# Kernel optimization log

Hardware: AMD Instinct MI355X
Metric: run time of the kernel (lower is better)

The kernel has to match this reference:

```python
import jax, jax.numpy as jnp
import numpy as np

EPS = 1e-12  # matches tf.nn.l2_normalize epsilon used by keras backend


def l2n(x, axis):
    return x / jnp.sqrt(jnp.maximum(jnp.sum(x * x, axis=axis, keepdims=True), EPS))


def setup_inputs() -> dict:
    key = jax.random.key(0)
    k1, k2, k3 = jax.random.split(key, 3)
    B, T, D, P = 32, 256, 512, 20
    inp_a = jax.random.normal(k1, (B, T, D), dtype=jnp.float32)
    inp_b = jax.random.normal(k2, (B, T, D), dtype=jnp.float32)
    # build(): output_dim weights of shape (1, D), 'uniform' init -> stacked (P, D)
    W = jax.random.uniform(k3, (P, D), dtype=jnp.float32, minval=-0.05, maxval=0.05)
    return {"inp_a": inp_a, "inp_b": inp_b, "W": W}


def reference(inp_a, inp_b, W):
    # l2-normalize over feature dim
    na = l2n(inp_a, -1)  # (B,T,D)
    nb = l2n(inp_b, -1)  # (B,T,D)
    # K.batch_dot(outp_b, outp_a, axes=[1,1]): contract seq axis -> (B,D,D)
    alpha = jnp.einsum('btd,bte->bde', nb, na)
    alpha = l2n(alpha, 1)
    # K.batch_dot(outp_b, alpha, axes=[2,1]): contract feature axis of b with axis1 of alpha -> (B,T,D)
    hmean = jnp.einsum('btd,bde->bte', nb, alpha)
    # per-perspective weighting + l2-normalize, vectorized over P perspectives
    aw = l2n(inp_a[:, :, None, :] * W[None, None, :, :], -1)   # (B,T,P,D)
    hw = l2n(hmean[:, :, None, :] * W[None, None, :, :], -1)   # (B,T,P,D)
    # batch_dot(hw_i, aw_i, axes=[2,2]) * eye summed == rowwise dot (diagonal only)
    persp = jnp.sum(aw * hw, axis=-1)  # (B,T,P)
    return (persp, persp)
```

## Files before the change

kernel.cpp:

```cpp
#include <hip/hip_runtime.h>
#include <hip/hip_bf16.h>

#define BB 32
#define TT 256
#define DD 512
#define PP 20
#define EPSF 1e-12f
#define BTP (BB * TT * PP)

typedef __attribute__((ext_vector_type(8))) short short8;
typedef __attribute__((ext_vector_type(4))) float f32x4;

__device__ inline unsigned short f2bf(float f) {
    unsigned u = __float_as_uint(f);
    u += 0x7fffu + ((u >> 16) & 1u);
    return (unsigned short)(u >> 16);
}
__device__ inline unsigned pk2(float lo, float hi) {
    __hip_bfloat162 h = __float22bfloat162_rn(float2{lo, hi});
    union { __hip_bfloat162 h; unsigned u; } c;
    c.h = h;
    return c.u;
}
__device__ inline float bf2f(unsigned s) {
    return __uint_as_float(s << 16);
}

union U8 { short8 s; uint4 u; };

__global__ __launch_bounds__(256)
void k_prep(const float* __restrict__ a, const float* __restrict__ b,
            const float* __restrict__ W,
            unsigned short* __restrict__ na_bf,
            unsigned short* __restrict__ nb_bf,
            float* __restrict__ q, unsigned short* __restrict__ W2) {
    const int row  = blockIdx.x * 4 + (threadIdx.x >> 6);
    const int lane = threadIdx.x & 63;
    const float4* pa = (const float4*)(a + (size_t)row * DD);
    const float4* pb = (const float4*)(b + (size_t)row * DD);
    float4 a0 = pa[2 * lane], a1 = pa[2 * lane + 1];
    float4 b0 = pb[2 * lane], b1 = pb[2 * lane + 1];
    float sa = a0.x * a0.x + a0.y * a0.y + a0.z * a0.z + a0.w * a0.w
             + a1.x * a1.x + a1.y * a1.y + a1.z * a1.z + a1.w * a1.w;
    float sb = b0.x * b0.x + b0.y * b0.y + b0.z * b0.z + b0.w * b0.w
             + b1.x * b1.x + b1.y * b1.y + b1.z * b1.z + b1.w * b1.w;
#pragma unroll
    for (int off = 1; off < 64; off <<= 1) {
        sa += __shfl_xor(sa, off);
        sb += __shfl_xor(sb, off);
    }
    const float ia_ = rsqrtf(fmaxf(sa, EPSF));
    const float ib_ = rsqrtf(fmaxf(sb, EPSF));
    uint4 oa, ob;
    oa.x = pk2(a0.x * ia_, a0.y * ia_);
    oa.y = pk2(a0.z * ia_, a0.w * ia_);
    oa.z = pk2(a1.x * ia_, a1.y * ia_);
    oa.w = pk2(a1.z * ia_, a1.w * ia_);
    ob.x = pk2(b0.x * ib_, b0.y * ib_);
    ob.y = pk2(b0.z * ib_, b0.w * ib_);
    ob.z = pk2(b1.x * ib_, b1.y * ib_);
    ob.w = pk2(b1.z * ib_, b1.w * ib_);
    *(uint4*)(na_bf + (size_t)row * DD + 8 * lane) = oa;
    *(uint4*)(nb_bf + (size_t)row * DD + 8 * lane) = ob;
    if (lane < 2) {
        const int i2 = 2 * row + lane;
        q[i2] = 0.f;
        const float w = (i2 < PP * DD) ? W[i2] : 0.f;
        W2[i2] = f2bf(w * w);
    }
}

__global__ __launch_bounds__(256)
void k_gemm_g(const unsigned short* __restrict__ nb,
              unsigned short* __restrict__ G) {
    const int bz  = blockIdx.z;
    const int tid = threadIdx.x;
    const int t0 = blockIdx.y * 64;
    const int s0 = blockIdx.x * 64;
    __shared__ __align__(16) unsigned short As[64 * 40];
    __shared__ __align__(16) unsigned short Bs[64 * 40];

    const int wave = tid >> 6, lane = tid & 63;
    const int quad = lane >> 4, ln = lane & 15;
    const int wm = wave >> 1, wn = wave & 1;

    const unsigned short* nbb = nb + (size_t)bz * TT * DD;

    const int lr = tid >> 2;
    const int c8 = (tid & 3) * 8;

    f32x4 acc[2][2];
#pragma unroll
    for (int i = 0; i < 2; ++i)
#pragma unroll
        for (int j = 0; j < 2; ++j)
#pragma unroll
            for (int r = 0; r < 4; ++r) acc[i][j][r] = 0.f;

    for (int k0 = 0; k0 < DD; k0 += 32) {
        *(uint4*)&As[lr * 40 + c8] =
            *(const uint4*)(nbb + (size_t)(t0 + lr) * DD + k0 + c8);
        *(uint4*)&Bs[lr * 40 + c8] =
            *(const uint4*)(nbb + (size_t)(s0 + lr) * DD + k0 + c8);
        __syncthreads();
        short8 af[2], bf[2];
        af[0] = *(const short8*)&As[(wm * 32 + ln) * 40 + quad * 8];
        af[1] = *(const short8*)&As[(wm * 32 + 16 + ln) * 40 + quad * 8];
        bf[0] = *(const short8*)&Bs[(wn * 32 + ln) * 40 + quad * 8];
        bf[1] = *(const short8*)&Bs[(wn * 32 + 16 + ln) * 40 + quad * 8];
#pragma unroll
        for (int i = 0; i < 2; ++i)
#pragma unroll
            for (int j = 0; j < 2; ++j)
                acc[i][j] = __builtin_amdgcn_mfma_f32_16x16x32_bf16(
                    af[i], bf[j], acc[i][j], 0, 0, 0);
        __syncthreads();
    }
    unsigned short* Gb = G + (size_t)bz * TT * TT;
#pragma unroll
    for (int i = 0; i < 2; ++i)
#pragma unroll
        for (int j = 0; j < 2; ++j) {
            const int col = s0 + wn * 32 + j * 16 + ln;
            const int row0 = t0 + wm * 32 + i * 16 + quad * 4;
#pragma unroll
            for (int r = 0; r < 4; r += 2) {
                const unsigned pk = pk2(acc[i][j][r], acc[i][j][r + 1]);
                Gb[(size_t)(row0 + r) * TT + col] = (unsigned short)pk;
                Gb[(size_t)(row0 + r + 1) * TT + col] = (unsigned short)(pk >> 16);
            }
        }
}

__global__ __launch_bounds__(256)
void k_gemm_h(const unsigned short* __restrict__ G,
              const unsigned short* __restrict__ na,
              unsigned short* __restrict__ H, float* __restrict__ q) {
    const int bz = blockIdx.z;
    const int t0 = blockIdx.y * 64;
    const int e0 = blockIdx.x * 64;
    __shared__ __align__(16) unsigned short As[64 * 40];
    __shared__ __align__(16) unsigned short Bs[64 * 40];
    __shared__ float qsum[64];

    const int tid  = threadIdx.x;
    const int wave = tid >> 6, lane = tid & 63;
    const int quad = lane >> 4, ln = lane & 15;
    const int wm = wave >> 1, wn = wave & 1;

    const unsigned short* Gb  = G  + (size_t)bz * TT * TT;
    const unsigned short* nab = na + (size_t)bz * TT * DD;

    const int lr = tid >> 2;
    const int c8 = (tid & 3) * 8;
    const int kr = tid >> 3;
    const int e8 = (tid & 7) * 8;

    f32x4 acc[2][2];
#pragma unroll
    for (int i = 0; i < 2; ++i)
#pragma unroll
        for (int j = 0; j < 2; ++j)
#pragma unroll
            for (int r = 0; r < 4; ++r) acc[i][j][r] = 0.f;

    for (int k0 = 0; k0 < TT; k0 += 32) {
        *(uint4*)&As[lr * 40 + c8] =
            *(const uint4*)(Gb + (size_t)(t0 + lr) * TT + k0 + c8);
        {
            uint4 v = *(const uint4*)(nab + (size_t)(k0 + kr) * DD + e0 + e8);
            Bs[(e8 + 0) * 40 + kr] = (unsigned short)(v.x);
            Bs[(e8 + 1) * 40 + kr] = (unsigned short)(v.x >> 16);
            Bs[(e8 + 2) * 40 + kr] = (unsigned short)(v.y);
            Bs[(e8 + 3) * 40 + kr] = (unsigned short)(v.y >> 16);
            Bs[(e8 + 4) * 40 + kr] = (unsigned short)(v.z);
            Bs[(e8 + 5) * 40 + kr] = (unsigned short)(v.z >> 16);
            Bs[(e8 + 6) * 40 + kr] = (unsigned short)(v.w);
            Bs[(e8 + 7) * 40 + kr] = (unsigned short)(v.w >> 16);
        }
        __syncthreads();
        short8 af[2], bf[2];
        af[0] = *(const short8*)&As[(wm * 32 + ln) * 40 + quad * 8];
        af[1] = *(const short8*)&As[(wm * 32 + 16 + ln) * 40 + quad * 8];
        bf[0] = *(const short8*)&Bs[(wn * 32 + ln) * 40 + quad * 8];
        bf[1] = *(const short8*)&Bs[(wn * 32 + 16 + ln) * 40 + quad * 8];
#pragma unroll
        for (int i = 0; i < 2; ++i)
#pragma unroll
            for (int j = 0; j < 2; ++j)
                acc[i][j] = __builtin_amdgcn_mfma_f32_16x16x32_bf16(
                    af[i], bf[j], acc[i][j], 0, 0, 0);
        __syncthreads();
    }

    if (tid < 64) qsum[tid] = 0.f;
    __syncthreads();

    unsigned short* Hb = H + (size_t)bz * TT * DD;
#pragma unroll
    for (int j = 0; j < 2; ++j) {
        const int col = e0 + wn * 32 + j * 16 + ln;
        float qp = 0.f;
#pragma unroll
        for (int i = 0; i < 2; ++i) {
            const int row0 = t0 + wm * 32 + i * 16 + quad * 4;
#pragma unroll
            for (int r = 0; r < 4; r += 2) {
                const float hv0 = acc[i][j][r];
                const float hv1 = acc[i][j][r + 1];
                const unsigned pk = pk2(hv0, hv1);
                Hb[(size_t)(row0 + r) * DD + col] = (unsigned short)pk;
                Hb[(size_t)(row0 + r + 1) * DD + col] = (unsigned short)(pk >> 16);
                qp = fmaf(bf2f(nab[(size_t)(row0 + r) * DD + col]), hv0, qp);
                qp = fmaf(bf2f(nab[(size_t)(row0 + r + 1) * DD + col]), hv1, qp);
            }
        }
        qp += __shfl_xor(qp, 16);
        qp += __shfl_xor(qp, 32);
        if (quad == 0) atomicAdd(&qsum[wn * 32 + j * 16 + ln], qp);
    }
    __syncthreads();
    if (tid < 64) atomicAdd(q + bz * DD + e0 + tid, qsum[tid]);
}

__global__ __launch_bounds__(128)
void k_persp_mfma(const unsigned short* __restrict__ na,
                  const unsigned short* __restrict__ H,
                  const float* __restrict__ q,
                  const unsigned short* __restrict__ W2,
                  float* __restrict__ out) {
    const int b    = blockIdx.y;
    const int r0   = blockIdx.x * 16;
    const int wave = threadIdx.x >> 6;
    const int lane = threadIdx.x & 63;
    const int quad = lane >> 4, ln = lane & 15;
    const size_t rowbase = ((size_t)b * TT + r0 + ln) * DD;

    __shared__ float qs[DD];
    __shared__ float ps[64][24];
    {
        const float* qb = q + (size_t)b * DD;
        float4 v = *(const float4*)(qb + 4 * threadIdx.x);
        qs[4 * threadIdx.x + 0] = rsqrtf(fmaxf(v.x, EPSF));
        qs[4 * threadIdx.x + 1] = rsqrtf(fmaxf(v.y, EPSF));
        qs[4 * threadIdx.x + 2] = rsqrtf(fmaxf(v.z, EPSF));
        qs[4 * threadIdx.x + 3] = rsqrtf(fmaxf(v.w, EPSF));
    }
    __syncthreads();

    f32x4 s1[2], s2[2], s3[2];
#pragma unroll
    for (int j = 0; j < 2; ++j)
#pragma unroll
        for (int r = 0; r < 4; ++r) { s1[j][r] = 0.f; s2[j][r] = 0.f; s3[j][r] = 0.f; }

    const int kbeg = wave * 256;
    for (int k0 = kbeg; k0 < kbeg + 256; k0 += 32) {
        const int k = k0 + quad * 8;
        uint4 au = *(const uint4*)(na + rowbase + k);
        uint4 hu = *(const uint4*)(H + rowbase + k);
        float4 q0 = *(const float4*)&qs[k];
        float4 q1 = *(const float4*)&qs[k + 4];
        const float av[8] = {bf2f(au.x & 0xffffu), bf2f(au.x >> 16),
                             bf2f(au.y & 0xffffu), bf2f(au.y >> 16),
                             bf2f(au.z & 0xffffu), bf2f(au.z >> 16),
                             bf2f(au.w & 0xffffu), bf2f(au.w >> 16)};
        const float qv[8] = {q0.x, q0.y, q0.z, q0.w, q1.x, q1.y, q1.z, q1.w};
        float hv[8] = {bf2f(hu.x & 0xffffu), bf2f(hu.x >> 16),
                       bf2f(hu.y & 0xffffu), bf2f(hu.y >> 16),
                       bf2f(hu.z & 0xffffu), bf2f(hu.z >> 16),
                       bf2f(hu.w & 0xffffu), bf2f(hu.w >> 16)};
#pragma unroll
        for (int t = 0; t < 8; ++t) hv[t] *= qv[t];
        U8 ah, aa, hh;
        ah.u.x = pk2(av[0] * hv[0], av[1] * hv[1]);
        ah.u.y = pk2(av[2] * hv[2], av[3] * hv[3]);
        ah.u.z = pk2(av[4] * hv[4], av[5] * hv[5]);
        ah.u.w = pk2(av[6] * hv[6], av[7] * hv[7]);
        aa.u.x = pk2(av[0] * av[0], av[1] * av[1]);
        aa.u.y = pk2(av[2] * av[2], av[3] * av[3]);
        aa.u.z = pk2(av[4] * av[4], av[5] * av[5]);
        aa.u.w = pk2(av[6] * av[6], av[7] * av[7]);
        hh.u.x = pk2(hv[0] * hv[0], hv[1] * hv[1]);
        hh.u.y = pk2(hv[2] * hv[2], hv[3] * hv[3]);
        hh.u.z = pk2(hv[4] * hv[4], hv[5] * hv[5]);
        hh.u.w = pk2(hv[6] * hv[6], hv[7] * hv[7]);
        short8 bw0 = *(const short8*)(W2 + (size_t)ln * DD + k);
        short8 bw1 = *(const short8*)(W2 + (size_t)(16 + ln) * DD + k);
        s1[0] = __builtin_amdgcn_mfma_f32_16x16x32_bf16(ah.s, bw0, s1[0], 0, 0, 0);
        s1[1] = __builtin_amdgcn_mfma_f32_16x16x32_bf16(ah.s, bw1, s1[1], 0, 0, 0);
        s2[0] = __builtin_amdgcn_mfma_f32_16x16x32_bf16(aa.s, bw0, s2[0], 0, 0, 0);
        s2[1] = __builtin_amdgcn_mfma_f32_16x16x32_bf16(aa.s, bw1, s2[1], 0, 0, 0);
        s3[0] = __builtin_amdgcn_mfma_f32_16x16x32_bf16(hh.s, bw0, s3[0], 0, 0, 0);
        s3[1] = __builtin_amdgcn_mfma_f32_16x16x32_bf16(hh.s, bw1, s3[1], 0, 0, 0);
    }

    if (wave == 1) {
#pragma unroll
        for (int j = 0; j < 2; ++j)
#pragma unroll
            for (int r = 0; r < 4; ++r) {
                ps[lane][j * 4 + r]      = s1[j][r];
                ps[lane][8 + j * 4 + r]  = s2[j][r];
                ps[lane][16 + j * 4 + r] = s3[j][r];
            }
    }
    __syncthreads();
    if (wave == 0) {
#pragma unroll
        for (int j = 0; j < 2; ++j) {
            const int p = j * 16 + ln;
            if (p < PP) {
#pragma unroll
                for (int r = 0; r < 4; ++r) {
                    const float v1 = s1[j][r] + ps[lane][j * 4 + r];
                    const float v2 = s2[j][r] + ps[lane][8 + j * 4 + r];
                    const float v3 = s3[j][r] + ps[lane][16 + j * 4 + r];
                    const size_t row = (size_t)b * TT + r0 + quad * 4 + r;
                    const float v = v1 * rsqrtf(fmaxf(v2, EPSF))
                                       * rsqrtf(fmaxf(v3, EPSF));
                    out[row * PP + p] = v;
                    out[(size_t)BTP + row * PP + p] = v;
                }
            }
        }
    }
}

extern "C" void kernel_launch(void* const* d_in, const int* in_sizes, int n_in,
                              void* d_out, int out_size, void* d_ws, size_t ws_size,
                              hipStream_t stream) {
    (void)in_sizes; (void)n_in; (void)out_size; (void)ws_size;
    const float* a = (const float*)d_in[0];
    const float* b = (const float*)d_in[1];
    const float* W = (const float*)d_in[2];
    float* out = (float*)d_out;

    char* ws = (char*)d_ws;
    unsigned short* nb_bf = (unsigned short*)ws;
    unsigned short* na_bf = (unsigned short*)(ws + (8u << 20));
    unsigned short* G_bf  = (unsigned short*)(ws + (16u << 20));
    unsigned short* H_bf  = (unsigned short*)(ws + (20u << 20));
    float* q     = (float*)(ws + (28u << 20));
    unsigned short* W2 = (unsigned short*)(ws + (28u << 20) + (64u << 10));

    k_prep<<<BB * TT / 4, 256, 0, stream>>>(a, b, W, na_bf, nb_bf, q, W2);

    dim3 gG(4, 4, BB);
    k_gemm_g<<<gG, 256, 0, stream>>>(nb_bf, G_bf);

    dim3 gH(DD / 64, TT / 64, BB);
    k_gemm_h<<<gH, 256, 0, stream>>>(G_bf, na_bf, H_bf, q);

    dim3 gP(TT / 16, BB);
    k_persp_mfma<<<gP, 128, 0, stream>>>(na_bf, H_bf, q, W2, out);
}
```

Before: 111.7 us.

## Fuse four kernels into one cooperative persistent kernel with grid syncs

Merges the prep, two GEMM, and perspective kernels into a single cooperative kernel of 256 blocks. Grid-wide syncs replace the kernel boundaries, and each block loops over several tiles per phase. The aim is to remove three launch gaps and their tail effects. In exchange, parallelism drops to 256 blocks, which may underuse the 256 CUs with little latency hiding, and each grid.sync adds barrier cost.

New measurement: 235.5 us. +110.8%, slower.

```diff
diff --git a/kernel.cpp b/kernel.cpp
--- a/kernel.cpp
+++ b/kernel.cpp
@@ -1,5 +1,8 @@
 #include <hip/hip_runtime.h>
 #include <hip/hip_bf16.h>
+#include <hip/hip_cooperative_groups.h>
+
+namespace cg = cooperative_groups;
 
 #define BB 32
 #define TT 256
@@ -28,299 +31,308 @@
 
 union U8 { short8 s; uint4 u; };
 
+union SMem {
+    struct {
+        unsigned short As[64 * 40];
+        unsigned short Bs[64 * 40];
+        float qsum[64];
+    } g;
+    struct {
+        float qs[DD];
+        float ps[2][64][24];
+    } p;
+};
+
 __global__ __launch_bounds__(256)
-void k_prep(const float* __restrict__ a, const float* __restrict__ b,
+void k_mega(const float* __restrict__ a, const float* __restrict__ b,
             const float* __restrict__ W,
             unsigned short* __restrict__ na_bf,
             unsigned short* __restrict__ nb_bf,
-            float* __restrict__ q, unsigned short* __restrict__ W2) {
-    const int row  = blockIdx.x * 4 + (threadIdx.x >> 6);
-    const int lane = threadIdx.x & 63;
-    const float4* pa = (const float4*)(a + (size_t)row * DD);
-    const float4* pb = (const float4*)(b + (size_t)row * DD);
-    float4 a0 = pa[2 * lane], a1 = pa[2 * lane + 1];
-    float4 b0 = pb[2 * lane], b1 = pb[2 * lane + 1];
-    float sa = a0.x * a0.x + a0.y * a0.y + a0.z * a0.z + a0.w * a0.w
-             + a1.x * a1.x + a1.y * a1.y + a1.z * a1.z + a1.w * a1.w;
-    float sb = b0.x * b0.x + b0.y * b0.y + b0.z * b0.z + b0.w * b0.w
-             + b1.x * b1.x + b1.y * b1.y + b1.z * b1.z + b1.w * b1.w;
-#pragma unroll
-    for (int off = 1; off < 64; off <<= 1) {
-        sa += __shfl_xor(sa, off);
-        sb += __shfl_xor(sb, off);
+            unsigned short* __restrict__ G,
+            unsigned short* __restrict__ H,
+            float* __restrict__ q, unsigned short* __restrict__ W2,
+            float* __restrict__ out) {
+    __shared__ __align__(16) SMem sm;
+    cg::grid_group grid = cg::this_grid();
+
+    const int tid  = threadIdx.x;
+    const int wave = tid >> 6;
+    const int lane = tid & 63;
+    const int quad = lane >> 4, ln = lane & 15;
+
+    {
+        const int w = blockIdx.x * 4 + wave;
+#pragma unroll
+        for (int r8 = 0; r8 < 8; ++r8) {
+            const int row = w * 8 + r8;
+            const float4* pa = (const float4*)(a + (size_t)row * DD);
+            const float4* pb = (const float4*)(b + (size_t)row * DD);
+            float4 a0 = pa[2 * lane], a1 = pa[2 * lane + 1];
+            float4 b0 = pb[2 * lane], b1 = pb[2 * lane + 1];
+            float sa = a0.x * a0.x + a0.y * a0.y + a0.z * a0.z + a0.w * a0.w
+                     + a1.x * a1.x + a1.y * a1.y + a1.z * a1.z + a1.w * a1.w;
+            float sb = b0.x * b0.x + b0.y * b0.y + b0.z * b0.z + b0.w * b0.w
+                     + b1.x * b1.x + b1.y * b1.y + b1.z * b1.z + b1.w * b1.w;
+#pragma unroll
+            for (int off = 1; off < 64; off <<= 1) {
+                sa += __shfl_xor(sa, off);
+                sb += __shfl_xor(sb, off);
+            }
+            const float ia_ = rsqrtf(fmaxf(sa, EPSF));
+            const float ib_ = rsqrtf(fmaxf(sb, EPSF));
+            uint4 oa, ob;
+            oa.x = pk2(a0.x * ia_, a0.y * ia_);
+            oa.y = pk2(a0.z * ia_, a0.w * ia_);
+            oa.z = pk2(a1.x * ia_, a1.y * ia_);
+            oa.w = pk2(a1.z * ia_, a1.w * ia_);
+            ob.x = pk2(b0.x * ib_, b0.y * ib_);
+            ob.y = pk2(b0.z * ib_, b0.w * ib_);
+            ob.z = pk2(b1.x * ib_, b1.y * ib_);
+            ob.w = pk2(b1.z * ib_, b1.w * ib_);
+            *(uint4*)(na_bf + (size_t)row * DD + 8 * lane) = oa;
+            *(uint4*)(nb_bf + (size_t)row * DD + 8 * lane) = ob;
+            if (lane < 2) {
+                const int i2 = 2 * row + lane;
+                q[i2] = 0.f;
+                const float w2 = (i2 < PP * DD) ? W[i2] : 0.f;
+                W2[i2] = f2bf(w2 * w2);
+            }
+        }
     }
-    const float ia_ = rsqrtf(fmaxf(sa, EPSF));
-    const float ib_ = rsqrtf(fmaxf(sb, EPSF));
-    uint4 oa, ob;
-    oa.x = pk2(a0.x * ia_, a0.y * ia_);
-    oa.y = pk2(a0.z * ia_, a0.w * ia_);
-    oa.z = pk2(a1.x * ia_, a1.y * ia_);
-    oa.w = pk2(a1.z * ia_, a1.w * ia_);
-    ob.x = pk2(b0.x * ib_, b0.y * ib_);
-    ob.y = pk2(b0.z * ib_, b0.w * ib_);
-    ob.z = pk2(b1.x * ib_, b1.y * ib_);
-    ob.w = pk2(b1.z * ib_, b1.w * ib_);
-    *(uint4*)(na_bf + (size_t)row * DD + 8 * lane) = oa;
-    *(uint4*)(nb_bf + (size_t)row * DD + 8 * lane) = ob;
-    if (lane < 2) {
-        const int i2 = 2 * row + lane;
-        q[i2] = 0.f;
-        const float w = (i2 < PP * DD) ? W[i2] : 0.f;
-        W2[i2] = f2bf(w * w);
+    grid.sync();
+
+    {
+        const int wm = wave >> 1, wn = wave & 1;
+        const int lr = tid >> 2;
+        const int c8 = (tid & 3) * 8;
+#pragma unroll
+        for (int it = 0; it < 2; ++it) {
+            const int tt = blockIdx.x * 2 + it;
+            const int bz = tt >> 4;
+            const int t0 = ((tt >> 2) & 3) * 64;
+            const int s0 = (tt & 3) * 64;
+            const unsigned short* nbb = nb_bf + (size_t)bz * TT * DD;
+
+            f32x4 acc[2][2];
+#pragma unroll
+            for (int i = 0; i < 2; ++i)
+#pragma unroll
+                for (int j = 0; j < 2; ++j)
+#pragma unroll
+                    for (int r = 0; r < 4; ++r) acc[i][j][r] = 0.f;
+
+            for (int k0 = 0; k0 < DD; k0 += 32) {
+                *(uint4*)&sm.g.As[lr * 40 + c8] =
+                    *(const uint4*)(nbb + (size_t)(t0 + lr) * DD + k0 + c8);
+                *(uint4*)&sm.g.Bs[lr * 40 + c8] =
+                    *(const uint4*)(nbb + (size_t)(s0 + lr) * DD + k0 + c8);
+                __syncthreads();
+                short8 af[2], bf[2];
+                af[0] = *(const short8*)&sm.g.As[(wm * 32 + ln) * 40 + quad * 8];
+                af[1] = *(const short8*)&sm.g.As[(wm * 32 + 16 + ln) * 40 + quad * 8];
+                bf[0] = *(const short8*)&sm.g.Bs[(wn * 32 + ln) * 40 + quad * 8];
+                bf[1] = *(const short8*)&sm.g.Bs[(wn * 32 + 16 + ln) * 40 + quad * 8];
+#pragma unroll
+                for (int i = 0; i < 2; ++i)
+#pragma unroll
+                    for (int j = 0; j < 2; ++j)
+                        acc[i][j] = __builtin_amdgcn_mfma_f32_16x16x32_bf16(
+                            af[i], bf[j], acc[i][j], 0, 0, 0);
+                __syncthreads();
+            }
+            unsigned short* Gb = G + (size_t)bz * TT * TT;
+#pragma unroll
+            for (int i = 0; i < 2; ++i)
+#pragma unroll
+                for (int j = 0; j < 2; ++j) {
+                    const int col = s0 + wn * 32 + j * 16 + ln;
+                    const int row0 = t0 + wm * 32 + i * 16 + quad * 4;
+#pragma unroll
+                    for (int r = 0; r < 4; r += 2) {
+                        const unsigned pk = pk2(acc[i][j][r], acc[i][j][r + 1]);
+                        Gb[(size_t)(row0 + r) * TT + col] = (unsigned short)pk;
+                        Gb[(size_t)(row0 + r + 1) * TT + col] = (unsigned short)(pk >> 16);
+                    }
+                }
+        }
     }
-}
-
-__global__ __launch_bounds__(256)
-void k_gemm_g(const unsigned short* __restrict__ nb,
-              unsigned short* __restrict__ G) {
-    const int bz  = blockIdx.z;
-    const int tid = threadIdx.x;
-    const int t0 = blockIdx.y * 64;
-    const int s0 = blockIdx.x * 64;
-    __shared__ __align__(16) unsigned short As[64 * 40];
-    __shared__ __align__(16) unsigned short Bs[64 * 40];
-
-    const int wave = tid >> 6, lane = tid & 63;
-    const int quad = lane >> 4, ln = lane & 15;
-    const int wm = wave >> 1, wn = wave & 1;
-
-    const unsigned short* nbb = nb + (size_t)bz * TT * DD;
-
-    const int lr = tid >> 2;
-    const int c8 = (tid & 3) * 8;
-
-    f32x4 acc[2][2];
-#pragma unroll
-    for (int i = 0; i < 2; ++i)
+    grid.sync();
+
+    {
+        const int wm = wave >> 1, wn = wave & 1;
+        const int lr = tid >> 2;
+        const int c8 = (tid & 3) * 8;
+        const int kr = tid >> 3;
+        const int e8 = (tid & 7) * 8;
+#pragma unroll
+        for (int it = 0; it < 4; ++it) {
+            const int tt = blockIdx.x * 4 + it;
+            const int bz = tt >> 5;
+            const int t0 = ((tt >> 3) & 3) * 64;
+            const int e0 = (tt & 7) * 64;
+            const unsigned short* Gb  = G     + (size_t)bz * TT * TT;
+            const unsigned short* nab = na_bf + (size_t)bz * TT * DD;
+
+            f32x4 acc[2][2];
+#pragma unroll
+            for (int i = 0; i < 2; ++i)
+#pragma unroll
+                for (int j = 0; j < 2; ++j)
+#pragma unroll
+                    for (int r = 0; r < 4; ++r) acc[i][j][r] = 0.f;
+
+            for (int k0 = 0; k0 < TT; k0 += 32) {
+                *(uint4*)&sm.g.As[lr * 40 + c8] =
+                    *(const uint4*)(Gb + (size_t)(t0 + lr) * TT + k0 + c8);
+                {
+                    uint4 v = *(const uint4*)(nab + (size_t)(k0 + kr) * DD + e0 + e8);
+                    sm.g.Bs[(e8 + 0) * 40 + kr] = (unsigned short)(v.x);
+                    sm.g.Bs[(e8 + 1) * 40 + kr] = (unsigned short)(v.x >> 16);
+                    sm.g.Bs[(e8 + 2) * 40 + kr] = (unsigned short)(v.y);
+                    sm.g.Bs[(e8 + 3) * 40 + kr] = (unsigned short)(v.y >> 16);
+                    sm.g.Bs[(e8 + 4) * 40 + kr] = (unsigned short)(v.z);
+                    sm.g.Bs[(e8 + 5) * 40 + kr] = (unsigned short)(v.z >> 16);
+                    sm.g.Bs[(e8 + 6) * 40 + kr] = (unsigned short)(v.w);
+                    sm.g.Bs[(e8 + 7) * 40 + kr] = (unsigned short)(v.w >> 16);
+                }
+                __syncthreads();
+                short8 af[2], bf[2];
+                af[0] = *(const short8*)&sm.g.As[(wm * 32 + ln) * 40 + quad * 8];
+                af[1] = *(const short8*)&sm.g.As[(wm * 32 + 16 + ln) * 40 + quad * 8];
+                bf[0] = *(const short8*)&sm.g.Bs[(wn * 32 + ln) * 40 + quad * 8];
+                bf[1] = *(const short8*)&sm.g.Bs[(wn * 32 + 16 + ln) * 40 + quad * 8];
+#pragma unroll
+                for (int i = 0; i < 2; ++i)
+#pragma unroll
+                    for (int j = 0; j < 2; ++j)
+                        acc[i][j] = __builtin_amdgcn_mfma_f32_16x16x32_bf16(
+                            af[i], bf[j], acc[i][j], 0, 0, 0);
+                __syncthreads();
+            }
+
+            if (tid < 64) sm.g.qsum[tid] = 0.f;
+            __syncthreads();
+
+            unsigned short* Hb = H + (size_t)bz * TT * DD;
+#pragma unroll
+            for (int j = 0; j < 2; ++j) {
+                const int col = e0 + wn * 32 + j * 16 + ln;
+                float qp = 0.f;
+#pragma unroll
+                for (int i = 0; i < 2; ++i) {
+                    const int row0 = t0 + wm * 32 + i * 16 + quad * 4;
+#pragma unroll
+                    for (int r = 0; r < 4; r += 2) {
+                        const float hv0 = acc[i][j][r];
+                        const float hv1 = acc[i][j][r + 1];
+                        const unsigned pk = pk2(hv0, hv1);
+                        Hb[(size_t)(row0 + r) * DD + col] = (unsigned short)pk;
+                        Hb[(size_t)(row0 + r + 1) * DD + col] = (unsigned short)(pk >> 16);
+                        qp = fmaf(bf2f(nab[(size_t)(row0 + r) * DD + col]), hv0, qp);
+                        qp = fmaf(bf2f(nab[(size_t)(row0 + r + 1) * DD + col]), hv1, qp);
+                    }
+                }
+                qp += __shfl_xor(qp, 16);
+                qp += __shfl_xor(qp, 32);
+                if (quad == 0) atomicAdd(&sm.g.qsum[wn * 32 + j * 16 + ln], qp);
+            }
+            __syncthreads();
+            if (tid < 64) atomicAdd(q + bz * DD + e0 + tid, sm.g.qsum[tid]);
+            __syncthreads();
+        }
+    }
+    grid.sync();
+
+    {
+        const int half = wave >> 1;
+        const int wv   = wave & 1;
+        const int tt   = blockIdx.x * 2 + half;
+        const int bb   = tt >> 4;
+        const int r0   = (tt & 15) * 16;
+        const size_t rowbase = ((size_t)bb * TT + r0 + ln) * DD;
+
+        {
+            const float* qb = q + (size_t)bb * DD;
+            float2 v = *(const float2*)(qb + 2 * tid);
+            sm.p.qs[2 * tid + 0] = rsqrtf(fmaxf(v.x, EPSF));
+            sm.p.qs[2 * tid + 1] = rsqrtf(fmaxf(v.y, EPSF));
+        }
+        __syncthreads();
+
+        f32x4 s1[2], s2[2], s3[2];
 #pragma unroll
         for (int j = 0; j < 2; ++j)
 #pragma unroll
-            for (int r = 0; r < 4; ++r) acc[i][j][r] = 0.f;
-
-    for (int k0 = 0; k0 < DD; k0 += 32) {
-        *(uint4*)&As[lr * 40 + c8] =
-            *(const uint4*)(nbb + (size_t)(t0 + lr) * DD + k0 + c8);
-        *(uint4*)&Bs[lr * 40 + c8] =
-            *(const uint4*)(nbb + (size_t)(s0 + lr) * DD + k0 + c8);
+            for (int r = 0; r < 4; ++r) { s1[j][r] = 0.f; s2[j][r] = 0.f; s3[j][r] = 0.f; }
+
+        const int kbeg = wv * 256;
+        for (int k0 = kbeg; k0 < kbeg + 256; k0 += 32) {
+            const int k = k0 + quad * 8;
+            uint4 au = *(const uint4*)(na_bf + rowbase + k);
+            uint4 hu = *(const uint4*)(H + rowbase + k);
+            float4 q0 = *(const float4*)&sm.p.qs[k];
+            float4 q1 = *(const float4*)&sm.p.qs[k + 4];
+            const float av[8] = {bf2f(au.x & 0xffffu), bf2f(au.x >> 16),
+                                 bf2f(au.y & 0xffffu), bf2f(au.y >> 16),
+                                 bf2f(au.z & 0xffffu), bf2f(au.z >> 16),
+                                 bf2f(au.w & 0xffffu), bf2f(au.w >> 16)};
+            const float qv[8] = {q0.x, q0.y, q0.z, q0.w, q1.x, q1.y, q1.z, q1.w};
+            float hv[8] = {bf2f(hu.x & 0xffffu), bf2f(hu.x >> 16),
+                           bf2f(hu.y & 0xffffu), bf2f(hu.y >> 16),
+                           bf2f(hu.z & 0xffffu), bf2f(hu.z >> 16),
+                           bf2f(hu.w & 0xffffu), bf2f(hu.w >> 16)};
+#pragma unroll
+            for (int t = 0; t < 8; ++t) hv[t] *= qv[t];
+            U8 ah, aa, hh;
+            ah.u.x = pk2(av[0] * hv[0], av[1] * hv[1]);
+            ah.u.y = pk2(av[2] * hv[2], av[3] * hv[3]);
+            ah.u.z = pk2(av[4] * hv[4], av[5] * hv[5]);
+            ah.u.w = pk2(av[6] * hv[6], av[7] * hv[7]);
+            aa.u.x = pk2(av[0] * av[0], av[1] * av[1]);
+            aa.u.y = pk2(av[2] * av[2], av[3] * av[3]);
+            aa.u.z = pk2(av[4] * av[4], av[5] * av[5]);
+            aa.u.w = pk2(av[6] * av[6], av[7] * av[7]);
+            hh.u.x = pk2(hv[0] * hv[0], hv[1] * hv[1]);
+            hh.u.y = pk2(hv[2] * hv[2], hv[3] * hv[3]);
+            hh.u.z = pk2(hv[4] * hv[4], hv[5] * hv[5]);
+            hh.u.w = pk2(hv[6] * hv[6], hv[7] * hv[7]);
+            short8 bw0 = *(const short8*)(W2 + (size_t)ln * DD + k);
+            short8 bw1 = *(const short8*)(W2 + (size_t)(16 + ln) * DD + k);
+            s1[0] = __builtin_amdgcn_mfma_f32_16x16x32_bf16(ah.s, bw0, s1[0], 0, 0, 0);
+            s1[1] = __builtin_amdgcn_mfma_f32_16x16x32_bf16(ah.s, bw1, s1[1], 0, 0, 0);
+            s2[0] = __builtin_amdgcn_mfma_f32_16x16x32_bf16(aa.s, bw0, s2[0], 0, 0, 0);
+            s2[1] = __builtin_amdgcn_mfma_f32_16x16x32_bf16(aa.s, bw1, s2[1], 0, 0, 0);
+            s3[0] = __builtin_amdgcn_mfma_f32_16x16x32_bf16(hh.s, bw0, s3[0], 0, 0, 0);
+            s3[1] = __builtin_amdgcn_mfma_f32_16x16x32_bf16(hh.s, bw1, s3[1], 0, 0, 0);
+        }
+
+        if (wv == 1) {
+#pragma unroll
+            for (int j = 0; j < 2; ++j)
+#pragma unroll
+                for (int r = 0; r < 4; ++r) {
+                    sm.p.ps[half][lane][j * 4 + r]      = s1[j][r];
+                    sm.p.ps[half][lane][8 + j * 4 + r]  = s2[j][r];
+                    sm.p.ps[half][lane][16 + j * 4 + r] = s3[j][r];
+                }
+        }
         __syncthreads();
-        short8 af[2], bf[2];
-        af[0] = *(const short8*)&As[(wm * 32 + ln) * 40 + quad * 8];
-        af[1] = *(const short8*)&As[(wm * 32 + 16 + ln) * 40 + quad * 8];
-        bf[0] = *(const short8*)&Bs[(wn * 32 + ln) * 40 + quad * 8];
-        bf[1] = *(const short8*)&Bs[(wn * 32 + 16 + ln) * 40 + quad * 8];
-#pragma unroll
-        for (int i = 0; i < 2; ++i)
-#pragma unroll
-            for (int j = 0; j < 2; ++j)
-                acc[i][j] = __builtin_amdgcn_mfma_f32_16x16x32_bf16(
-                    af[i], bf[j], acc[i][j], 0, 0, 0);
-        __syncthreads();
-    }
-    unsigned short* Gb = G + (size_t)bz * TT * TT;
-#pragma unroll
-    for (int i = 0; i < 2; ++i)
-#pragma unroll
-        for (int j = 0; j < 2; ++j) {
-            const int col = s0 + wn * 32 + j * 16 + ln;
-            const int row0 = t0 + wm * 32 + i * 16 + quad * 4;
-#pragma unroll
-            for (int r = 0; r < 4; r += 2) {
-                const unsigned pk = pk2(acc[i][j][r], acc[i][j][r + 1]);
-                Gb[(size_t)(row0 + r) * TT + col] = (unsigned short)pk;
-                Gb[(size_t)(row0 + r + 1) * TT + col] = (unsigned short)(pk >> 16);
-            }
-        }
-}
-
-__global__ __launch_bounds__(256)
-void k_gemm_h(const unsigned short* __restrict__ G,
-              const unsigned short* __restrict__ na,
-              unsigned short* __restrict__ H, float* __restrict__ q) {
-    const int bz = blockIdx.z;
-    const int t0 = blockIdx.y * 64;
-    const int e0 = blockIdx.x * 64;
-    __shared__ __align__(16) unsigned short As[64 * 40];
-    __shared__ __align__(16) unsigned short Bs[64 * 40];
-    __shared__ float qsum[64];
-
-    const int tid  = threadIdx.x;
-    const int wave = tid >> 6, lane = tid & 63;
-    const int quad = lane >> 4, ln = lane & 15;
-    const int wm = wave >> 1, wn = wave & 1;
-
-    const unsigned short* Gb  = G  + (size_t)bz * TT * TT;
-    const unsigned short* nab = na + (size_t)bz * TT * DD;
-
-    const int lr = tid >> 2;
-    const int c8 = (tid & 3) * 8;
-    const int kr = tid >> 3;
-    const int e8 = (tid & 7) * 8;
-
-    f32x4 acc[2][2];
-#pragma unroll
-    for (int i = 0; i < 2; ++i)
-#pragma unroll
-        for (int j = 0; j < 2; ++j)
-#pragma unroll
-            for (int r = 0; r < 4; ++r) acc[i][j][r] = 0.f;
-
-    for (int k0 = 0; k0 < TT; k0 += 32) {
-        *(uint4*)&As[lr * 40 + c8] =
-            *(const uint4*)(Gb + (size_t)(t0 + lr) * TT + k0 + c8);
-        {
-            uint4 v = *(const uint4*)(nab + (size_t)(k0 + kr) * DD + e0 + e8);
-            Bs[(e8 + 0) * 40 + kr] = (unsigned short)(v.x);
-            Bs[(e8 + 1) * 40 + kr] = (unsigned short)(v.x >> 16);
-            Bs[(e8 + 2) * 40 + kr] = (unsigned short)(v.y);
-            Bs[(e8 + 3) * 40 + kr] = (unsigned short)(v.y >> 16);
-            Bs[(e8 + 4) * 40 + kr] = (unsigned short)(v.z);
-            Bs[(e8 + 5) * 40 + kr] = (unsigned short)(v.z >> 16);
-            Bs[(e8 + 6) * 40 + kr] = (unsigned short)(v.w);
-            Bs[(e8 + 7) * 40 + kr] = (unsigned short)(v.w >> 16);
-        }
-        __syncthreads();
-        short8 af[2], bf[2];
-        af[0] = *(const short8*)&As[(wm * 32 + ln) * 40 + quad * 8];
-        af[1] = *(const short8*)&As[(wm * 32 + 16 + ln) * 40 + quad * 8];
-        bf[0] = *(const short8*)&Bs[(wn * 32 + ln) * 40 + quad * 8];
-        bf[1] = *(const short8*)&Bs[(wn * 32 + 16 + ln) * 40 + quad * 8];
-#pragma unroll
-        for (int i = 0; i < 2; ++i)
-#pragma unroll
-            for (int j = 0; j < 2; ++j)
-                acc[i][j] = __builtin_amdgcn_mfma_f32_16x16x32_bf16(
-                    af[i], bf[j], acc[i][j], 0, 0, 0);
-        __syncthreads();
-    }
-
-    if (tid < 64) qsum[tid] = 0.f;
-    __syncthreads();
-
-    unsigned short* Hb = H + (size_t)bz * TT * DD;
-#pragma unroll
-    for (int j = 0; j < 2; ++j) {
-        const int col = e0 + wn * 32 + j * 16 + ln;
-        float qp = 0.f;
-#pragma unroll
-        for (int i = 0; i < 2; ++i) {
-            const int row0 = t0 + wm * 32 + i * 16 + quad * 4;
-#pragma unroll
-            for (int r = 0; r < 4; r += 2) {
-                const float hv0 = acc[i][j][r];
-                const float hv1 = acc[i][j][r + 1];
-                const unsigned pk = pk2(hv0, hv1);
-                Hb[(size_t)(row0 + r) * DD + col] = (unsigned short)pk;
-                Hb[(size_t)(row0 + r + 1) * DD + col] = (unsigned short)(pk >> 16);
-                qp = fmaf(bf2f(nab[(size_t)(row0 + r) * DD + col]), hv0, qp);
-                qp = fmaf(bf2f(nab[(size_t)(row0 + r + 1) * DD + col]), hv1, qp);
-            }
-        }
-        qp += __shfl_xor(qp, 16);
-        qp += __shfl_xor(qp, 32);
-        if (quad == 0) atomicAdd(&qsum[wn * 32 + j * 16 + ln], qp);
-    }
-    __syncthreads();
-    if (tid < 64) atomicAdd(q + bz * DD + e0 + tid, qsum[tid]);
-}
-
-__global__ __launch_bounds__(128)
-void k_persp_mfma(const unsigned short* __restrict__ na,
-                  const unsigned short* __restrict__ H,
-                  const float* __restrict__ q,
-                  const unsigned short* __restrict__ W2,
-                  float* __restrict__ out) {
-    const int b    = blockIdx.y;
-    const int r0   = blockIdx.x * 16;
-    const int wave = threadIdx.x >> 6;
-    const int lane = threadIdx.x & 63;
-    const int quad = lane >> 4, ln = lane & 15;
-    const size_t rowbase = ((size_t)b * TT + r0 + ln) * DD;
-
-    __shared__ float qs[DD];
-    __shared__ float ps[64][24];
-    {
-        const float* qb = q + (size_t)b * DD;
-        float4 v = *(const float4*)(qb + 4 * threadIdx.x);
-        qs[4 * threadIdx.x + 0] = rsqrtf(fmaxf(v.x, EPSF));
-        qs[4 * threadIdx.x + 1] = rsqrtf(fmaxf(v.y, EPSF));
-        qs[4 * threadIdx.x + 2] = rsqrtf(fmaxf(v.z, EPSF));
-        qs[4 * threadIdx.x + 3] = rsqrtf(fmaxf(v.w, EPSF));
-    }
-    __syncthreads();
-
-    f32x4 s1[2], s2[2], s3[2];
-#pragma unroll
-    for (int j = 0; j < 2; ++j)
-#pragma unroll
-        for (int r = 0; r < 4; ++r) { s1[j][r] = 0.f; s2[j][r] = 0.f; s3[j][r] = 0.f; }
-
-    const int kbeg = wave * 256;
-    for (int k0 = kbeg; k0 < kbeg + 256; k0 += 32) {
-        const int k = k0 + quad * 8;
-        uint4 au = *(const uint4*)(na + rowbase + k);
-        uint4 hu = *(const uint4*)(H + rowbase + k);
-        float4 q0 = *(const float4*)&qs[k];
-        float4 q1 = *(const float4*)&qs[k + 4];
-        const float av[8] = {bf2f(au.x & 0xffffu), bf2f(au.x >> 16),
-                             bf2f(au.y & 0xffffu), bf2f(au.y >> 16),
-                             bf2f(au.z & 0xffffu), bf2f(au.z >> 16),
-                             bf2f(au.w & 0xffffu), bf2f(au.w >> 16)};
-        const float qv[8] = {q0.x, q0.y, q0.z, q0.w, q1.x, q1.y, q1.z, q1.w};
-        float hv[8] = {bf2f(hu.x & 0xffffu), bf2f(hu.x >> 16),
-                       bf2f(hu.y & 0xffffu), bf2f(hu.y >> 16),
-                       bf2f(hu.z & 0xffffu), bf2f(hu.z >> 16),
-                       bf2f(hu.w & 0xffffu), bf2f(hu.w >> 16)};
-#pragma unroll
-        for (int t = 0; t < 8; ++t) hv[t] *= qv[t];
-        U8 ah, aa, hh;
-        ah.u.x = pk2(av[0] * hv[0], av[1] * hv[1]);
-        ah.u.y = pk2(av[2] * hv[2], av[3] * hv[3]);
-        ah.u.z = pk2(av[4] * hv[4], av[5] * hv[5]);
-        ah.u.w = pk2(av[6] * hv[6], av[7] * hv[7]);
-        aa.u.x = pk2(av[0] * av[0], av[1] * av[1]);
-        aa.u.y = pk2(av[2] * av[2], av[3] * av[3]);
-        aa.u.z = pk2(av[4] * av[4], av[5] * av[5]);
-        aa.u.w = pk2(av[6] * av[6], av[7] * av[7]);
-        hh.u.x = pk2(hv[0] * hv[0], hv[1] * hv[1]);
-        hh.u.y = pk2(hv[2] * hv[2], hv[3] * hv[3]);
-        hh.u.z = pk2(hv[4] * hv[4], hv[5] * hv[5]);
-        hh.u.w = pk2(hv[6] * hv[6], hv[7] * hv[7]);
-        short8 bw0 = *(const short8*)(W2 + (size_t)ln * DD + k);
-        short8 bw1 = *(const short8*)(W2 + (size_t)(16 + ln) * DD + k);
-        s1[0] = __builtin_amdgcn_mfma_f32_16x16x32_bf16(ah.s, bw0, s1[0], 0, 0, 0);
-        s1[1] = __builtin_amdgcn_mfma_f32_16x16x32_bf16(ah.s, bw1, s1[1], 0, 0, 0);
-        s2[0] = __builtin_amdgcn_mfma_f32_16x16x32_bf16(aa.s, bw0, s2[0], 0, 0, 0);
-        s2[1] = __builtin_amdgcn_mfma_f32_16x16x32_bf16(aa.s, bw1, s2[1], 0, 0, 0);
-        s3[0] = __builtin_amdgcn_mfma_f32_16x16x32_bf16(hh.s, bw0, s3[0], 0, 0, 0);
-        s3[1] = __builtin_amdgcn_mfma_f32_16x16x32_bf16(hh.s, bw1, s3[1], 0, 0, 0);
-    }
-
-    if (wave == 1) {
-#pragma unroll
-        for (int j = 0; j < 2; ++j)
-#pragma unroll
-            for (int r = 0; r < 4; ++r) {
-                ps[lane][j * 4 + r]      = s1[j][r];
-                ps[lane][8 + j * 4 + r]  = s2[j][r];
-                ps[lane][16 + j * 4 + r] = s3[j][r];
-            }
-    }
-    __syncthreads();
-    if (wave == 0) {
-#pragma unroll
-        for (int j = 0; j < 2; ++j) {
-            const int p = j * 16 + ln;
-            if (p < PP) {
-#pragma unroll
-                for (int r = 0; r < 4; ++r) {
-                    const float v1 = s1[j][r] + ps[lane][j * 4 + r];
-                    const float v2 = s2[j][r] + ps[lane][8 + j * 4 + r];
-                    const float v3 = s3[j][r] + ps[lane][16 + j * 4 + r];
-                    const size_t row = (size_t)b * TT + r0 + quad * 4 + r;
-                    const float v = v1 * rsqrtf(fmaxf(v2, EPSF))
-                                       * rsqrtf(fmaxf(v3, EPSF));
-                    out[row * PP + p] = v;
-                    out[(size_t)BTP + row * PP + p] = v;
+        if (wv == 0) {
+#pragma unroll
+            for (int j = 0; j < 2; ++j) {
+                const int p = j * 16 + ln;
+                if (p < PP) {
+#pragma unroll
+                    for (int r = 0; r < 4; ++r) {
+                        const float v1 = s1[j][r] + sm.p.ps[half][lane][j * 4 + r];
+                        const float v2 = s2[j][r] + sm.p.ps[half][lane][8 + j * 4 + r];
+                        const float v3 = s3[j][r] + sm.p.ps[half][lane][16 + j * 4 + r];
+                        const size_t row = (size_t)bb * TT + r0 + quad * 4 + r;
+                        const float v = v1 * rsqrtf(fmaxf(v2, EPSF))
+                                           * rsqrtf(fmaxf(v3, EPSF));
+                        out[row * PP + p] = v;
+                        out[(size_t)BTP + row * PP + p] = v;
+                    }
                 }
             }
         }
@@ -344,14 +356,9 @@
     float* q     = (float*)(ws + (28u << 20));
     unsigned short* W2 = (unsigned short*)(ws + (28u << 20) + (64u << 10));
 
-    k_prep<<<BB * TT / 4, 256, 0, stream>>>(a, b, W, na_bf, nb_bf, q, W2);
-
-    dim3 gG(4, 4, BB);
-    k_gemm_g<<<gG, 256, 0, stream>>>(nb_bf, G_bf);
-
-    dim3 gH(DD / 64, TT / 64, BB);
-    k_gemm_h<<<gH, 256, 0, stream>>>(G_bf, na_bf, H_bf, q);
-
-    dim3 gP(TT / 16, BB);
-    k_persp_mfma<<<gP, 128, 0, stream>>>(na_bf, H_bf, q, W2, out);
-}
+    void* args[] = {(void*)&a, (void*)&b, (void*)&W,
+                    (void*)&na_bf, (void*)&nb_bf, (void*)&G_bf, (void*)&H_bf,
+                    (void*)&q, (void*)&W2, (void*)&out};
+    hipLaunchCooperativeKernel((const void*)k_mega, dim3(256), dim3(256),
+                               args, 0, stream);
+}
```
